# Kernel optimization log

Hardware: AMD Instinct MI355X
Metric: run time of the kernel (lower is better)

## Reference

```python
import jax, jax.numpy as jnp
import numpy as np

B, S, H = 2, 2048, 2304
NH, HD, NKV = 8, 256, 4
WINDOW = 512
CAP = 50.0
THETA = 10000.0
NEG_INF = -2.3819763e38


def setup_inputs() -> dict:
    key = jax.random.key(0)
    ks = jax.random.split(key, 6)
    hidden_states = jax.random.normal(ks[0], (B, S, H), dtype=jnp.float32)
    # causal additive mask (0 where attend, -inf-ish where masked)
    i = jnp.arange(S)
    causal = i[None, :] <= i[:, None]
    attention_mask = jnp.broadcast_to(
        jnp.where(causal, 0.0, NEG_INF).astype(jnp.float32)[None, None], (B, 1, S, S)
    )
    position_ids = jnp.broadcast_to(jnp.arange(S, dtype=jnp.int32)[None], (B, S))
    scale = 0.02
    Wq = jax.random.normal(ks[1], (H, NH * HD), dtype=jnp.float32) * scale
    Wk = jax.random.normal(ks[2], (H, NKV * HD), dtype=jnp.float32) * scale
    Wv = jax.random.normal(ks[3], (H, NKV * HD), dtype=jnp.float32) * scale
    Wo = jax.random.normal(ks[4], (NH * HD, H), dtype=jnp.float32) * scale
    return {
        "hidden_states": hidden_states,
        "attention_mask": attention_mask,
        "position_ids": position_ids,
        "Wq": Wq,
        "Wk": Wk,
        "Wv": Wv,
        "Wo": Wo,
    }


def _rotate_half(x):
    h = x.shape[-1] // 2
    return jnp.concatenate([-x[..., h:], x[..., :h]], axis=-1)


def reference(hidden_states, attention_mask, position_ids, Wq, Wk, Wv, Wo):
    b, s, _ = hidden_states.shape
    q = (hidden_states @ Wq).reshape(b, s, NH, HD).transpose(0, 2, 1, 3)   # [B,NH,S,HD]
    k = (hidden_states @ Wk).reshape(b, s, NKV, HD).transpose(0, 2, 1, 3)  # [B,NKV,S,HD]
    v = (hidden_states @ Wv).reshape(b, s, NKV, HD).transpose(0, 2, 1, 3)
    # rotary embedding
    inv_freq = 1.0 / (THETA ** (jnp.arange(0, HD, 2, dtype=jnp.float32) / HD))
    freqs = position_ids.astype(jnp.float32)[..., None] * inv_freq  # [B,S,HD/2]
    emb = jnp.concatenate([freqs, freqs], axis=-1)                  # [B,S,HD]
    cos = jnp.cos(emb)[:, None]  # unsqueeze head dim
    sin = jnp.sin(emb)[:, None]
    q = q * cos + _rotate_half(q) * sin
    k = k * cos + _rotate_half(k) * sin
    # GQA: repeat kv heads
    rep = NH // NKV
    k = jnp.repeat(k, rep, axis=1)
    v = jnp.repeat(v, rep, axis=1)
    logits = jnp.einsum("bhqd,bhkd->bhqk", q, k) / jnp.sqrt(jnp.float32(HD))
    # sliding-window mask: keep |i-j| <= WINDOW-1, else NEG_INF
    idx = jnp.arange(s)
    sliding = jnp.abs(idx[:, None] - idx[None, :]) <= (WINDOW - 1)
    mask = jnp.where(sliding[None, None], attention_mask, NEG_INF)
    # tanh logit softcapping, then additive mask
    logits = jnp.tanh(logits / CAP) * CAP + mask
    probs = jax.nn.softmax(logits.astype(jnp.float32), axis=-1).astype(q.dtype)
    out = jnp.einsum("bhqk,bhkd->bhqd", probs, v)
    out = out.transpose(0, 2, 1, 3).reshape(b, s, NH * HD)
    return out @ Wo
```

## Files before the change

kernel.cpp:

```cpp
#include <hip/hip_runtime.h>
#include <cmath>

#define B_   2
#define S_   2048
#define H_   2304
#define NH_  8
#define HD_  256
#define NKV_ 4
#define WIN_ 512
#define QKVW 4096

typedef unsigned short ushort_t;
typedef __attribute__((ext_vector_type(8))) short bf16x8;
typedef __attribute__((ext_vector_type(4))) float floatx4;

__device__ __forceinline__ unsigned short f2bf(float f) {
  unsigned u = __builtin_bit_cast(unsigned, f);
  u += 0x7fff + ((u >> 16) & 1);
  return (unsigned short)(u >> 16);
}
__device__ __forceinline__ float bf2f(ushort_t v) {
  unsigned u = (unsigned)v << 16;
  return __builtin_bit_cast(float, u);
}

__device__ __forceinline__ void gl2lds16(const void* g, void* l) {
  __builtin_amdgcn_global_load_lds(
      (const __attribute__((address_space(1))) unsigned int*)g,
      (__attribute__((address_space(3))) unsigned int*)l, 16, 0, 0);
}

__global__ void cast_bf16(const float* __restrict__ in, ushort_t* __restrict__ out) {
  const int i = blockIdx.x * 256 + threadIdx.x;
  float4 v = ((const float4*)in)[i];
  ushort4 o;
  o.x = f2bf(v.x); o.y = f2bf(v.y); o.z = f2bf(v.z); o.w = f2bf(v.w);
  ((ushort4*)out)[i] = o;
}

__global__ void transpose_cast(const float* __restrict__ W, ushort_t* __restrict__ Wt,
                               int K, int N) {
  __shared__ float t[32][33];
  const int lx = threadIdx.x & 31, ly = threadIdx.x >> 5;
  const int n0 = blockIdx.x * 32, k0 = blockIdx.y * 32;
#pragma unroll
  for (int i = 0; i < 4; ++i)
    t[ly + i * 8][lx] = W[(long long)(k0 + ly + i * 8) * N + n0 + lx];
  __syncthreads();
#pragma unroll
  for (int i = 0; i < 4; ++i)
    Wt[(long long)(n0 + ly + i * 8) * K + k0 + lx] = f2bf(t[lx][ly + i * 8]);
}

#define LDA_FROM(base_, qm_) do { \
  _Pragma("unroll") for (int i_ = 0; i_ < 4; ++i_) { \
    const int row_ = wm + (qm_) * 64 + i_ * 16 + l15; \
    _Pragma("unroll") for (int kk_ = 0; kk_ < 2; ++kk_) \
      aR[i_][kk_] = *(const bf16x8*)&(base_)[row_ * 64 + (((kk_ * 4 + lq) ^ (l15 & 7)) * 8)]; \
  } \
} while (0)

#define LDB_FROM(base_, dst_, qn_) do { \
  _Pragma("unroll") for (int j_ = 0; j_ < 2; ++j_) { \
    const int row_ = wn + (qn_) * 32 + j_ * 16 + l15; \
    _Pragma("unroll") for (int kk_ = 0; kk_ < 2; ++kk_) \
      dst_[j_][kk_] = *(const bf16x8*)&(base_)[row_ * 64 + (((kk_ * 4 + lq) ^ (l15 & 7)) * 8)]; \
  } \
} while (0)

#define MFMA_QUAD(qm_, qn_, breg_) do { \
  _Pragma("unroll") for (int kk_ = 0; kk_ < 2; ++kk_) \
  _Pragma("unroll") for (int i_ = 0; i_ < 4; ++i_) \
  _Pragma("unroll") for (int j_ = 0; j_ < 2; ++j_) \
    acc[(qm_) * 4 + i_][(qn_) * 2 + j_] = __builtin_amdgcn_mfma_f32_16x16x32_bf16( \
        aR[i_][kk_], breg_[j_][kk_], acc[(qm_) * 4 + i_][(qn_) * 2 + j_], 0, 0, 0); \
} while (0)

#define STAGE_A(dst_, gsrc_, t_, qm_) do { \
  _Pragma("unroll") for (int jj_ = 0; jj_ < 2; ++jj_) { \
    const int g_ = w * 2 + jj_; \
    const int tr0_ = ((g_ >> 3) * 128) + (qm_) * 64 + (g_ & 7) * 8; \
    gl2lds16(gsrc_ + (size_t)tr0_ * K + (size_t)(t_) * 64 + laneOff, dst_ + tr0_ * 64); \
  } \
} while (0)

#define STAGE_B(dst_, gsrc_, t_, qn_) do { \
  _Pragma("unroll") for (int jj_ = 0; jj_ < 2; ++jj_) { \
    const int g_ = w * 2 + jj_; \
    const int tr0_ = ((g_ >> 2) * 64) + (qn_) * 32 + (g_ & 3) * 8; \
    gl2lds16(gsrc_ + (size_t)tr0_ * K + (size_t)(t_) * 64 + laneOff, dst_ + tr0_ * 64); \
  } \
} while (0)

#define SB0() __builtin_amdgcn_sched_barrier(0)
#define LGKM0() do { asm volatile("s_waitcnt lgkmcnt(0)" ::: "memory"); SB0(); } while (0)

template <bool OUT_BF16>
__launch_bounds__(512)
__global__ void gemm_8ph(const ushort_t* __restrict__ A,
                         const ushort_t* __restrict__ Bt,
                         void* __restrict__ Cv, int M, int N, int K) {
  extern __shared__ __attribute__((aligned(128))) ushort_t smem[];
  const int tid = threadIdx.x, lane = tid & 63, w = tid >> 6;
  const int wm = (w >> 2) * 128, wn = (w & 3) * 64;
  const int l15 = lane & 15, lq = lane >> 4;

  const int nwg  = gridDim.x * gridDim.y;
  const int orig = blockIdx.y * gridDim.x + blockIdx.x;
  const int cpx  = nwg >> 3;
  const int swz  = (orig & 7) * cpx + (orig >> 3);
  const int bx   = swz % gridDim.x, by = swz / gridDim.x;
  const int bm = by * 256, bn = bx * 256;
  const int NT = K >> 6;

  const ushort_t* Ab = A + (size_t)bm * K;
  const ushort_t* Bb = Bt + (size_t)bn * K;
  const size_t laneOff = (size_t)(lane >> 3) * K + (size_t)(((lane & 7) ^ (lane >> 3)) * 8);

  ushort_t* A0s = smem;
  ushort_t* B0s = smem + 16384;
  ushort_t* A1s = smem + 32768;
  ushort_t* B1s = smem + 49152;

  floatx4 acc[8][4] = {};
  bf16x8 aR[4][2], b0[2][2], b1[2][2];

  STAGE_A(A0s, Ab, 0, 0);
  STAGE_B(B0s, Bb, 0, 0);
  STAGE_B(B0s, Bb, 0, 1);
  STAGE_A(A0s, Ab, 0, 1);
  if (NT > 1) {
    STAGE_A(A1s, Ab, 1, 0);
    STAGE_B(B1s, Bb, 1, 0);
    STAGE_B(B1s, Bb, 1, 1);
    asm volatile("s_waitcnt vmcnt(6)" ::: "memory");
  } else {
    asm volatile("s_waitcnt vmcnt(0)" ::: "memory");
  }
  __builtin_amdgcn_s_barrier();
  LDA_FROM(A0s, 0);
  LDB_FROM(B0s, b0, 0);

  for (int t = 0; t < NT; ++t) {
    ushort_t* ldsA  = (t & 1) ? A1s : A0s;
    ushort_t* ldsB  = (t & 1) ? B1s : B0s;
    ushort_t* ldsAo = (t & 1) ? A0s : A1s;
    ushort_t* ldsBo = (t & 1) ? B0s : B1s;

    LGKM0();
    if (t + 1 < NT) STAGE_A(ldsAo, Ab, t + 1, 1);
    __builtin_amdgcn_s_setprio(1);
    MFMA_QUAD(0, 0, b0);
    __builtin_amdgcn_s_setprio(0);
    SB0();
    LDB_FROM(ldsB, b1, 1);
    __builtin_amdgcn_s_barrier();

    LGKM0();
    if (t + 2 < NT) STAGE_A(ldsA, Ab, t + 2, 0);
    __builtin_amdgcn_s_setprio(1);
    MFMA_QUAD(0, 1, b1);
    __builtin_amdgcn_s_setprio(0);
    SB0();
    LDA_FROM(ldsA, 1);
    __builtin_amdgcn_s_barrier();

    LGKM0();
    if (t + 2 < NT) STAGE_B(ldsB, Bb, t + 2, 0);
    __builtin_amdgcn_s_setprio(1);
    MFMA_QUAD(1, 1, b1);
    __builtin_amdgcn_s_setprio(0);
    SB0();
    if (t + 1 < NT) {
      if (t == NT - 2) asm volatile("s_waitcnt vmcnt(0)" ::: "memory");
      else             asm volatile("s_waitcnt vmcnt(4)" ::: "memory");
    }
    __builtin_amdgcn_s_barrier();

    if (t + 2 < NT) STAGE_B(ldsB, Bb, t + 2, 1);
    __builtin_amdgcn_s_setprio(1);
    MFMA_QUAD(1, 0, b0);
    __builtin_amdgcn_s_setprio(0);
    SB0();
    if (t + 1 < NT) {
      LDA_FROM(ldsAo, 0);
      LDB_FROM(ldsBo, b0, 0);
    }
    __builtin_amdgcn_s_barrier();
  }

  const int r0 = lq * 4;
#pragma unroll
  for (int mf = 0; mf < 8; ++mf)
#pragma unroll
    for (int nf = 0; nf < 4; ++nf) {
      const long long base = (long long)(bm + wm + mf * 16 + r0) * N + bn + wn + nf * 16 + l15;
      if (OUT_BF16) {
        ushort_t* Cp = (ushort_t*)Cv + base;
#pragma unroll
        for (int rr = 0; rr < 4; ++rr) Cp[(long long)rr * N] = f2bf(acc[mf][nf][rr]);
      } else {
        float* Cp = (float*)Cv + base;
#pragma unroll
        for (int rr = 0; rr < 4; ++rr) Cp[(long long)rr * N] = acc[mf][nf][rr];
      }
    }
}

#undef LDA_FROM
#undef LDB_FROM
#undef MFMA_QUAD
#undef STAGE_A
#undef STAGE_B

template <bool OUT_BF16>
__launch_bounds__(256)
__global__ void gemm_bt(const ushort_t* __restrict__ A,
                        const ushort_t* __restrict__ Bt,
                        void* __restrict__ Cv, int M, int N, int K) {
  __shared__ ushort_t As[128 * 64];
  __shared__ ushort_t Bs[128 * 64];
  const int tid = threadIdx.x, lane = tid & 63, wid = tid >> 6;
  const int bm = blockIdx.y * 128, bn = blockIdx.x * 128;
  const int wm = (wid >> 1) * 64, wn = (wid & 1) * 64;

  floatx4 acc[4][4] = {};

  const int r  = tid >> 1;
  const int cp = (tid & 1) * 4;
  const int wkey = r & 7;
  const ushort_t* Ap = A  + (long long)(bm + r) * K + cp * 8;
  const ushort_t* Bp = Bt + (long long)(bn + r) * K + cp * 8;
  ushort_t* Aw = &As[r * 64];
  ushort_t* Bw = &Bs[r * 64];

  const int l15 = lane & 15, lq = lane >> 4;
  const int rkey = l15 & 7;

  bf16x8 ar[4], br[4];
#pragma unroll
  for (int i = 0; i < 4; ++i) {
    ar[i] = *(const bf16x8*)(Ap + i * 8);
    br[i] = *(const bf16x8*)(Bp + i * 8);
  }

  for (int k0 = 0; k0 < K; k0 += 64) {
    __syncthreads();
#pragma unroll
    for (int i = 0; i < 4; ++i) {
      *(bf16x8*)&Aw[((cp + i) ^ wkey) * 8] = ar[i];
      *(bf16x8*)&Bw[((cp + i) ^ wkey) * 8] = br[i];
    }
    __syncthreads();

    if (k0 + 64 < K) {
      const int kn = k0 + 64;
#pragma unroll
      for (int i = 0; i < 4; ++i) {
        ar[i] = *(const bf16x8*)(Ap + kn + i * 8);
        br[i] = *(const bf16x8*)(Bp + kn + i * 8);
      }
    }

#pragma unroll
    for (int kk = 0; kk < 2; ++kk) {
      bf16x8 af[4], bfr[4];
#pragma unroll
      for (int i = 0; i < 4; ++i) {
        af[i]  = *(const bf16x8*)&As[(wm + i * 16 + l15) * 64 + ((kk * 4 + lq) ^ rkey) * 8];
        bfr[i] = *(const bf16x8*)&Bs[(wn + i * 16 + l15) * 64 + ((kk * 4 + lq) ^ rkey) * 8];
      }
#pragma unroll
      for (int i = 0; i < 4; ++i)
#pragma unroll
        for (int j = 0; j < 4; ++j)
          acc[i][j] = __builtin_amdgcn_mfma_f32_16x16x32_bf16(af[i], bfr[j], acc[i][j], 0, 0, 0);
    }
  }

  const int r0 = lq * 4, c0 = l15;
#pragma unroll
  for (int i = 0; i < 4; ++i)
#pragma unroll
    for (int j = 0; j < 4; ++j) {
      const long long base = (long long)(bm + wm + i * 16 + r0) * N + bn + wn + j * 16 + c0;
      if (OUT_BF16) {
        ushort_t* Cp = (ushort_t*)Cv + base;
#pragma unroll
        for (int rr = 0; rr < 4; ++rr) Cp[(long long)rr * N] = f2bf(acc[i][j][rr]);
      } else {
        float* Cp = (float*)Cv + base;
#pragma unroll
        for (int rr = 0; rr < 4; ++rr) Cp[(long long)rr * N] = acc[i][j][rr];
      }
    }
}

__global__ void rope_inplace(ushort_t* __restrict__ QKV16, const int* __restrict__ pos) {
  const int bs  = blockIdx.x;
  const int gid = blockIdx.y * 256 + threadIdx.x;
  const int head = gid >> 7;
  const int d    = gid & 127;
  const float pp   = (float)pos[bs];
  const float invf = __expf(-(float)d * (9.210340371976184f / 128.0f));
  const float ang  = pp * invf;
  const float cc = cosf(ang), sn = sinf(ang);
  ushort_t* base = QKV16 + (size_t)bs * QKVW + head * HD_;
  const float x1 = bf2f(base[d]);
  const float x2 = bf2f(base[d + 128]);
  float o1 = x1 * cc - x2 * sn;
  float o2 = x2 * cc + x1 * sn;
  if (head < NH_) { o1 *= 0.0625f; o2 *= 0.0625f; }
  base[d]       = f2bf(o1);
  base[d + 128] = f2bf(o2);
}

__global__ void v_prep(const ushort_t* __restrict__ QKV16, ushort_t* __restrict__ Vt16) {
  __shared__ ushort_t tile[32][33];
  const int k0 = blockIdx.x * 32, d0 = blockIdx.y * 32;
  const int b = blockIdx.z >> 2, hk = blockIdx.z & 3;
  const int lx = threadIdx.x & 31, ly = threadIdx.x >> 5;
#pragma unroll
  for (int i = 0; i < 4; ++i)
    tile[ly + 8 * i][lx] =
        QKV16[(size_t)(b * S_ + k0 + ly + 8 * i) * QKVW + 3072 + hk * HD_ + d0 + lx];
  __syncthreads();
#pragma unroll
  for (int i = 0; i < 4; ++i)
    Vt16[((size_t)(b * NKV_ + hk) * HD_ + d0 + ly + 8 * i) * S_ + k0 + lx] =
        tile[lx][ly + 8 * i];
}

__launch_bounds__(512)
__global__ void attn_mfma(const ushort_t* __restrict__ QKV16,
                          const ushort_t* __restrict__ Vt16,
                          ushort_t* __restrict__ AOb) {
  __shared__ ushort_t Ks[32 * 256];
  __shared__ ushort_t Vts[256 * 32];
  __shared__ ushort_t Ps[8][16 * 32];
  __shared__ float rsb[8][16];

  const int lane = threadIdx.x & 63, w = threadIdx.x >> 6;
  const int l15 = lane & 15, lq = lane >> 4;
  const int qb = blockIdx.x * 64;
  const int hp = blockIdx.y, b = blockIdx.z;
  const int h  = hp * 2 + (w >> 2);
  const int hw = w & 3;

  const ushort_t* Qh = QKV16 + (size_t)b * S_ * QKVW + h * HD_;
  const ushort_t* Kh = QKV16 + (size_t)b * S_ * QKVW + 2048 + hp * HD_;
  const ushort_t* Vh = Vt16 + ((size_t)(b * NKV_ + hp) * HD_) * S_;

  const int qw = qb + hw * 16;

  bf16x8 afq[8];
  {
    const ushort_t* qr = Qh + (size_t)(qw + l15) * QKVW + lq * 8;
#pragma unroll
    for (int kd = 0; kd < 8; ++kd) afq[kd] = *(const bf16x8*)(qr + kd * 32);
  }

  floatx4 acc[16] = {};
  float rs[4] = {0.f, 0.f, 0.f, 0.f};

  int kb0 = qb - (WIN_ - 1);
  if (kb0 < 0) kb0 = 0;
  kb0 &= ~31;

  const int ksp = lane & 31, ksr = lane >> 5;
  const int vsp = lane & 3,  vsr = lane >> 2;

  for (int kb = kb0; kb < qb + 64; kb += 32) {
    __syncthreads();
#pragma unroll
    for (int i = 0; i < 2; ++i) {
      const int kl = w * 4 + 2 * i + ksr;
      gl2lds16(Kh + (size_t)(kb + kl) * QKVW + (ksp ^ (kl & 31)) * 8,
               &Ks[(w * 4 + 2 * i) * 256]);
    }
#pragma unroll
    for (int i = 0; i < 2; ++i) {
      const int dl = w * 32 + 16 * i + vsr;
      gl2lds16(Vh + (size_t)dl * S_ + kb + (vsp ^ ((dl >> 1) & 3)) * 8,
               &Vts[(w * 32 + 16 * i) * 32]);
    }
    __syncthreads();

    if (kb <= qw + 15 && kb + 31 >= qw - (WIN_ - 1)) {
      ushort_t* Pw = Ps[w];
#pragma unroll
      for (int kt = 0; kt < 2; ++kt) {
        floatx4 sacc = {};
        const int keyl = kt * 16 + l15;
        const int krow = keyl * 256;
        const int ksw = keyl & 31;
#pragma unroll
        for (int kd = 0; kd < 8; ++kd) {
          bf16x8 bk = *(const bf16x8*)&Ks[krow + ((kd * 4 + lq) ^ ksw) * 8];
          sacc = __builtin_amdgcn_mfma_f32_16x16x32_bf16(afq[kd], bk, sacc, 0, 0, 0);
        }
        const int keyg = kb + keyl;
#pragma unroll
        for (int rr = 0; rr < 4; ++rr) {
          const int qg = qw + lq * 4 + rr;
          const float t = __expf(sacc[rr] * 0.04f);
          const float L = 50.f - __fdividef(100.f, t + 1.f);
          float p = __expf(L);
          p = (keyg <= qg && keyg >= qg - (WIN_ - 1)) ? p : 0.f;
          rs[rr] += p;
          const int ql = lq * 4 + rr;
          const int ch = kt * 2 + (l15 >> 3);
          Pw[ql * 32 + ((ch ^ ((ql >> 1) & 3)) * 8) + (l15 & 7)] = f2bf(p);
        }
      }
      asm volatile("s_waitcnt lgkmcnt(0)" ::: "memory");

      const bf16x8 bp = *(const bf16x8*)&Pw[l15 * 32 + ((lq ^ ((l15 >> 1) & 3)) * 8)];
      const int vsw = (l15 >> 1) & 3;
#pragma unroll
      for (int t = 0; t < 16; ++t) {
        bf16x8 av = *(const bf16x8*)&Vts[(t * 16 + l15) * 32 + ((lq ^ vsw) * 8)];
        acc[t] = __builtin_amdgcn_mfma_f32_16x16x32_bf16(av, bp, acc[t], 0, 0, 0);
      }
    }
  }

#pragma unroll
  for (int rr = 0; rr < 4; ++rr) {
    rs[rr] += __shfl_xor(rs[rr], 1, 64);
    rs[rr] += __shfl_xor(rs[rr], 2, 64);
    rs[rr] += __shfl_xor(rs[rr], 4, 64);
    rs[rr] += __shfl_xor(rs[rr], 8, 64);
  }
  if (l15 == 0) {
#pragma unroll
    for (int rr = 0; rr < 4; ++rr) rsb[w][lq * 4 + rr] = rs[rr];
  }
  asm volatile("s_waitcnt lgkmcnt(0)" ::: "memory");
  __builtin_amdgcn_wave_barrier();
  const float inv = 1.0f / rsb[w][l15];

  const size_t ob = ((size_t)(b * S_ + qw + l15) * NH_ + h) * HD_;
#pragma unroll
  for (int t = 0; t < 16; ++t) {
    ushort4 o;
    o.x = f2bf(acc[t][0] * inv);
    o.y = f2bf(acc[t][1] * inv);
    o.z = f2bf(acc[t][2] * inv);
    o.w = f2bf(acc[t][3] * inv);
    *(ushort4*)&AOb[ob + t * 16 + lq * 4] = o;
  }
}

extern "C" void kernel_launch(void* const* d_in, const int* in_sizes, int n_in,
                              void* d_out, int out_size, void* d_ws, size_t ws_size,
                              hipStream_t stream) {
  const float* X   = (const float*)d_in[0];
  const int*   pos = (const int*)d_in[2];
  const float* Wq  = (const float*)d_in[3];
  const float* Wk  = (const float*)d_in[4];
  const float* Wv  = (const float*)d_in[5];
  const float* Wo  = (const float*)d_in[6];
  float* out = (float*)d_out;

  const int M  = B_ * S_;
  const int NQ = NH_ * HD_;
  const int NK = NKV_ * HD_;

  char* w = (char*)d_ws;
  ushort_t* QKV16 = (ushort_t*)w;  w += (size_t)M * QKVW * 2;
  ushort_t* Xb    = (ushort_t*)w;  w += (size_t)M * H_ * 2;
  ushort_t* Wqkvt = (ushort_t*)w;  w += (size_t)QKVW * H_ * 2;
  ushort_t* Wot   = (ushort_t*)w;  w += (size_t)H_ * NQ * 2;
  ushort_t* Vt16  = (ushort_t*)w;  w += (size_t)B_ * NKV_ * S_ * HD_ * 2;
  ushort_t* AOb   = (ushort_t*)w;  w += (size_t)M * NQ * 2;

  static bool g_init = false, g_8ph_ok = false;
  if (!g_init) {
    hipError_t e1 = hipFuncSetAttribute(
        reinterpret_cast<const void*>(&gemm_8ph<true>),
        hipFuncAttributeMaxDynamicSharedMemorySize, 131072);
    hipError_t e2 = hipFuncSetAttribute(
        reinterpret_cast<const void*>(&gemm_8ph<false>),
        hipFuncAttributeMaxDynamicSharedMemorySize, 131072);
    g_8ph_ok = (e1 == hipSuccess && e2 == hipSuccess);
    g_init = true;
  }

  dim3 blk(256);

  cast_bf16<<<(M * H_) / 1024, blk, 0, stream>>>(X, Xb);
  transpose_cast<<<dim3(NQ / 32, H_ / 32), blk, 0, stream>>>(Wq, Wqkvt, H_, NQ);
  transpose_cast<<<dim3(NK / 32, H_ / 32), blk, 0, stream>>>(Wk, Wqkvt + (size_t)2048 * H_, H_, NK);
  transpose_cast<<<dim3(NK / 32, H_ / 32), blk, 0, stream>>>(Wv, Wqkvt + (size_t)3072 * H_, H_, NK);
  transpose_cast<<<dim3(H_ / 32, NQ / 32), blk, 0, stream>>>(Wo, Wot, NQ, H_);

  if (g_8ph_ok) {
    gemm_8ph<true><<<dim3(QKVW / 256, M / 256), dim3(512), 131072, stream>>>(
        Xb, Wqkvt, QKV16, M, QKVW, H_);
  } else {
    gemm_bt<true><<<dim3(QKVW / 128, M / 128), blk, 0, stream>>>(Xb, Wqkvt, QKV16, M, QKVW, H_);
  }

  rope_inplace<<<dim3(M, 6), blk, 0, stream>>>(QKV16, pos);
  v_prep<<<dim3(S_ / 32, HD_ / 32, B_ * NKV_), blk, 0, stream>>>(QKV16, Vt16);

  attn_mfma<<<dim3(S_ / 64, NKV_, B_), dim3(512), 0, stream>>>(QKV16, Vt16, AOb);

  if (g_8ph_ok) {
    gemm_8ph<false><<<dim3(H_ / 256, M / 256), dim3(512), 131072, stream>>>(
        AOb, Wot, out, M, H_, NQ);
  } else {
    gemm_bt<false><<<dim3(H_ / 128, M / 128), blk, 0, stream>>>(AOb, Wot, out, M, H_, NQ);
  }
}
```

Baseline: 357.3 us.

## Unroll GEMM main loop by two with double-buffered fragment registers and fast sincos

Restructures the 8-phase bf16 GEMM main loop to process two K-tiles per iteration. It keeps two register sets each for the A and B fragments, so LDS reads for the next quadrant are issued ahead of the MFMAs that consume the current set. The explicit lgkmcnt waits and sched barriers are removed, leaving the compiler to insert LDS waits, and setprio is folded into the MFMA macro. The loop now assumes an even tile count and relies more on compiler scheduling, and uses more registers. The RoPE kernel also switches to the fast __sincosf intrinsic, which trades accuracy at large angles for cheaper trig.

```diff
diff --git a/kernel.cpp b/kernel.cpp
--- a/kernel.cpp
+++ b/kernel.cpp
@@ -52,15 +52,15 @@
     Wt[(long long)(n0 + ly + i * 8) * K + k0 + lx] = f2bf(t[lx][ly + i * 8]);
 }
 
-#define LDA_FROM(base_, qm_) do { \
+#define LDA_SET(dst_, base_, qm_) do { \
   _Pragma("unroll") for (int i_ = 0; i_ < 4; ++i_) { \
     const int row_ = wm + (qm_) * 64 + i_ * 16 + l15; \
     _Pragma("unroll") for (int kk_ = 0; kk_ < 2; ++kk_) \
-      aR[i_][kk_] = *(const bf16x8*)&(base_)[row_ * 64 + (((kk_ * 4 + lq) ^ (l15 & 7)) * 8)]; \
+      dst_[i_][kk_] = *(const bf16x8*)&(base_)[row_ * 64 + (((kk_ * 4 + lq) ^ (l15 & 7)) * 8)]; \
   } \
 } while (0)
 
-#define LDB_FROM(base_, dst_, qn_) do { \
+#define LDB_SET(dst_, base_, qn_) do { \
   _Pragma("unroll") for (int j_ = 0; j_ < 2; ++j_) { \
     const int row_ = wn + (qn_) * 32 + j_ * 16 + l15; \
     _Pragma("unroll") for (int kk_ = 0; kk_ < 2; ++kk_) \
@@ -68,12 +68,14 @@
   } \
 } while (0)
 
-#define MFMA_QUAD(qm_, qn_, breg_) do { \
+#define MFMA_Q(qm_, qn_, aset_, bset_) do { \
+  __builtin_amdgcn_s_setprio(1); \
   _Pragma("unroll") for (int kk_ = 0; kk_ < 2; ++kk_) \
   _Pragma("unroll") for (int i_ = 0; i_ < 4; ++i_) \
   _Pragma("unroll") for (int j_ = 0; j_ < 2; ++j_) \
     acc[(qm_) * 4 + i_][(qn_) * 2 + j_] = __builtin_amdgcn_mfma_f32_16x16x32_bf16( \
-        aR[i_][kk_], breg_[j_][kk_], acc[(qm_) * 4 + i_][(qn_) * 2 + j_], 0, 0, 0); \
+        aset_[i_][kk_], bset_[j_][kk_], acc[(qm_) * 4 + i_][(qn_) * 2 + j_], 0, 0, 0); \
+  __builtin_amdgcn_s_setprio(0); \
 } while (0)
 
 #define STAGE_A(dst_, gsrc_, t_, qm_) do { \
@@ -92,8 +94,8 @@
   } \
 } while (0)
 
-#define SB0() __builtin_amdgcn_sched_barrier(0)
-#define LGKM0() do { asm volatile("s_waitcnt lgkmcnt(0)" ::: "memory"); SB0(); } while (0)
+#define BAR()  asm volatile("s_barrier" ::: "memory")
+#define VM(n_) asm volatile("s_waitcnt vmcnt(" #n_ ")" ::: "memory")
 
 template <bool OUT_BF16>
 __launch_bounds__(512)
@@ -117,76 +119,74 @@
   const ushort_t* Bb = Bt + (size_t)bn * K;
   const size_t laneOff = (size_t)(lane >> 3) * K + (size_t)(((lane & 7) ^ (lane >> 3)) * 8);
 
-  ushort_t* A0s = smem;
-  ushort_t* B0s = smem + 16384;
-  ushort_t* A1s = smem + 32768;
-  ushort_t* B1s = smem + 49152;
+  ushort_t* Ae = smem;
+  ushort_t* Ao = smem + 16384;
+  ushort_t* Be = smem + 32768;
+  ushort_t* Bo = smem + 49152;
 
   floatx4 acc[8][4] = {};
-  bf16x8 aR[4][2], b0[2][2], b1[2][2];
-
-  STAGE_A(A0s, Ab, 0, 0);
-  STAGE_B(B0s, Bb, 0, 0);
-  STAGE_B(B0s, Bb, 0, 1);
-  STAGE_A(A0s, Ab, 0, 1);
+  bf16x8 aA[4][2], aB[4][2], bA[2][2], bB[2][2];
+
+  STAGE_A(Ae, Ab, 0, 0);
+  STAGE_B(Be, Bb, 0, 0);
+  STAGE_B(Be, Bb, 0, 1);
+  STAGE_A(Ae, Ab, 0, 1);
   if (NT > 1) {
-    STAGE_A(A1s, Ab, 1, 0);
-    STAGE_B(B1s, Bb, 1, 0);
-    STAGE_B(B1s, Bb, 1, 1);
-    asm volatile("s_waitcnt vmcnt(6)" ::: "memory");
+    STAGE_A(Ao, Ab, 1, 0);
+    STAGE_B(Bo, Bb, 1, 0);
+    STAGE_B(Bo, Bb, 1, 1);
+    VM(6);
   } else {
-    asm volatile("s_waitcnt vmcnt(0)" ::: "memory");
-  }
-  __builtin_amdgcn_s_barrier();
-  LDA_FROM(A0s, 0);
-  LDB_FROM(B0s, b0, 0);
-
-  for (int t = 0; t < NT; ++t) {
-    ushort_t* ldsA  = (t & 1) ? A1s : A0s;
-    ushort_t* ldsB  = (t & 1) ? B1s : B0s;
-    ushort_t* ldsAo = (t & 1) ? A0s : A1s;
-    ushort_t* ldsBo = (t & 1) ? B0s : B1s;
-
-    LGKM0();
-    if (t + 1 < NT) STAGE_A(ldsAo, Ab, t + 1, 1);
-    __builtin_amdgcn_s_setprio(1);
-    MFMA_QUAD(0, 0, b0);
-    __builtin_amdgcn_s_setprio(0);
-    SB0();
-    LDB_FROM(ldsB, b1, 1);
-    __builtin_amdgcn_s_barrier();
-
-    LGKM0();
-    if (t + 2 < NT) STAGE_A(ldsA, Ab, t + 2, 0);
-    __builtin_amdgcn_s_setprio(1);
-    MFMA_QUAD(0, 1, b1);
-    __builtin_amdgcn_s_setprio(0);
-    SB0();
-    LDA_FROM(ldsA, 1);
-    __builtin_amdgcn_s_barrier();
-
-    LGKM0();
-    if (t + 2 < NT) STAGE_B(ldsB, Bb, t + 2, 0);
-    __builtin_amdgcn_s_setprio(1);
-    MFMA_QUAD(1, 1, b1);
-    __builtin_amdgcn_s_setprio(0);
-    SB0();
-    if (t + 1 < NT) {
-      if (t == NT - 2) asm volatile("s_waitcnt vmcnt(0)" ::: "memory");
-      else             asm volatile("s_waitcnt vmcnt(4)" ::: "memory");
-    }
-    __builtin_amdgcn_s_barrier();
-
-    if (t + 2 < NT) STAGE_B(ldsB, Bb, t + 2, 1);
-    __builtin_amdgcn_s_setprio(1);
-    MFMA_QUAD(1, 0, b0);
-    __builtin_amdgcn_s_setprio(0);
-    SB0();
-    if (t + 1 < NT) {
-      LDA_FROM(ldsAo, 0);
-      LDB_FROM(ldsBo, b0, 0);
-    }
-    __builtin_amdgcn_s_barrier();
+    VM(0);
+  }
+  BAR();
+  LDA_SET(aA, Ae, 0);
+  LDB_SET(bA, Be, 0);
+
+  for (int t = 0; t < NT; t += 2) {
+    LDB_SET(bB, Be, 1);
+    LDA_SET(aB, Ae, 1);
+    STAGE_A(Ao, Ab, t + 1, 1);
+    MFMA_Q(0, 0, aA, bA);
+    BAR();
+
+    if (t + 2 < NT) STAGE_A(Ae, Ab, t + 2, 0);
+    MFMA_Q(0, 1, aA, bB);
+    BAR();
+
+    if (t + 2 < NT) STAGE_B(Be, Bb, t + 2, 0);
+    MFMA_Q(1, 1, aB, bB);
+    if (t + 2 < NT) { VM(4); } else { VM(0); }
+    BAR();
+
+    LDA_SET(aA, Ao, 0);
+    LDB_SET(bB, Bo, 1);
+    if (t + 2 < NT) STAGE_B(Be, Bb, t + 2, 1);
+    MFMA_Q(1, 0, aB, bA);
+    BAR();
+
+    LDB_SET(bA, Bo, 0);
+    LDA_SET(aB, Ao, 1);
+    if (t + 2 < NT) STAGE_A(Ae, Ab, t + 2, 1);
+    MFMA_Q(0, 1, aA, bB);
+    BAR();
+
+    if (t + 3 < NT) STAGE_A(Ao, Ab, t + 3, 0);
+    MFMA_Q(0, 0, aA, bA);
+    BAR();
+
+    if (t + 3 < NT) STAGE_B(Bo, Bb, t + 3, 0);
+    MFMA_Q(1, 0, aB, bA);
+    if (t + 2 < NT) { VM(4); }
+    BAR();
+
+    if (t + 2 < NT) {
+      LDA_SET(aA, Ae, 0);
+      LDB_SET(bA, Be, 0);
+    }
+    if (t + 3 < NT) STAGE_B(Bo, Bb, t + 3, 1);
+    MFMA_Q(1, 1, aB, bB);
+    BAR();
   }
 
   const int r0 = lq * 4;
@@ -207,11 +207,13 @@
     }
 }
 
-#undef LDA_FROM
-#undef LDB_FROM
-#undef MFMA_QUAD
+#undef LDA_SET
+#undef LDB_SET
+#undef MFMA_Q
 #undef STAGE_A
 #undef STAGE_B
+#undef BAR
+#undef VM
 
 template <bool OUT_BF16>
 __launch_bounds__(256)
@@ -304,7 +306,8 @@
   const float pp   = (float)pos[bs];
   const float invf = __expf(-(float)d * (9.210340371976184f / 128.0f));
   const float ang  = pp * invf;
-  const float cc = cosf(ang), sn = sinf(ang);
+  float sn, cc;
+  __sincosf(ang, &sn, &cc);
   ushort_t* base = QKV16 + (size_t)bs * QKVW + head * HD_;
   const float x1 = bf2f(base[d]);
   const float x2 = bf2f(base[d + 128]);
```

Result: slower. 629.6 us (+76.2%).
